# Optimization experiments

Hardware: AMD Instinct MI355X
Metric: run time of the kernel (lower is better)

The kernel has to match this reference:

```python
import jax, jax.numpy as jnp
import numpy as np

B, S, D = 2, 1024, 4096
HQ, HKV, HD = 32, 8, 128
GROUPS = HQ // HKV          # 4
SCALE = HD ** -0.5


def _rope_tables(key):
    # standard RoPE cos/sin tables, non-interleaved (half-split) layout
    inv_freq = 1.0 / (10000.0 ** (jnp.arange(0, HD, 2, dtype=jnp.float32) / HD))  # [HD/2]
    pos = jnp.arange(S, dtype=jnp.float32)                                        # [S]
    freqs = pos[:, None] * inv_freq[None, :]                                      # [S, HD/2]
    emb = jnp.concatenate([freqs, freqs], axis=-1)                                # [S, HD]
    cos = jnp.broadcast_to(jnp.cos(emb)[None], (B, S, HD))
    sin = jnp.broadcast_to(jnp.sin(emb)[None], (B, S, HD))
    return cos, sin


def setup_inputs() -> dict:
    key = jax.random.key(0)
    ks = jax.random.split(key, 6)
    hidden_states = jax.random.normal(ks[0], (B, S, D), dtype=jnp.float32)
    cos_table, sin_table = _rope_tables(ks[1])
    Wq = jax.random.normal(ks[2], (D, HQ * HD), dtype=jnp.float32) * (D ** -0.5)
    Wk = jax.random.normal(ks[3], (D, HKV * HD), dtype=jnp.float32) * (D ** -0.5)
    Wv = jax.random.normal(ks[4], (D, HKV * HD), dtype=jnp.float32) * (D ** -0.5)
    Wo = jax.random.normal(ks[5], (HQ * HD, D), dtype=jnp.float32) * ((HQ * HD) ** -0.5)
    return {"hidden_states": hidden_states, "cos_table": cos_table,
            "sin_table": sin_table, "Wq": Wq, "Wk": Wk, "Wv": Wv, "Wo": Wo}


def _rotate_half(x):
    x1, x2 = jnp.split(x, 2, axis=-1)
    return jnp.concatenate([-x2, x1], axis=-1)


def _apply_rope(x, cos, sin):
    # x: [B, S, H, HD]; cos/sin: [B, S, HD] broadcast across heads
    c = cos[:, :, None, :]
    s = sin[:, :, None, :]
    return x * c + _rotate_half(x) * s


def reference(hidden_states, cos_table, sin_table, Wq, Wk, Wv, Wo):
    b, s, _ = hidden_states.shape
    # QKV projections (no bias, Llama-style)
    q = (hidden_states @ Wq).reshape(b, s, HQ, HD)
    k = (hidden_states @ Wk).reshape(b, s, HKV, HD)
    v = (hidden_states @ Wv).reshape(b, s, HKV, HD)
    # fused RoPE on q and k (in [B, S, H, HD] layout, as in source)
    q = _apply_rope(q, cos_table, sin_table)
    k = _apply_rope(k, cos_table, sin_table)
    # -> [B, H, S, HD]
    q = q.transpose(0, 2, 1, 3)
    k = k.transpose(0, 2, 1, 3)
    v = v.transpose(0, 2, 1, 3)
    # GQA repeat_kv: [B, HKV, S, HD] -> [B, HQ, S, HD]
    k = jnp.repeat(k, GROUPS, axis=1)
    v = jnp.repeat(v, GROUPS, axis=1)
    # SDPA, no mask (source calls sdpa without a mask)
    scores = jnp.einsum('bhqd,bhkd->bhqk', q, k) * SCALE
    attn = jax.nn.softmax(scores, axis=-1)
    out = jnp.einsum('bhqk,bhkd->bhqd', attn, v)
    out = out.transpose(0, 2, 1, 3).reshape(b, s, HQ * HD)
    return out @ Wo
```

## Files before the change

### kernel.cpp

```cpp
#include <hip/hip_runtime.h>

#define B_   2
#define S_   1024
#define D_   4096
#define HQ_  32
#define HKV_ 8
#define HD_  128
#define SCALE_ 0.08838834764831845f

typedef unsigned short u16;
typedef __attribute__((ext_vector_type(8))) short s16x8;
typedef __attribute__((ext_vector_type(4))) short s16x4;
typedef __attribute__((ext_vector_type(4))) float f32x4;

#define MFMA(a,b,c) __builtin_amdgcn_mfma_f32_16x16x32_bf16((a),(b),(c),0,0,0)

__device__ __forceinline__ u16 bf16_rne(float x) {
  unsigned u = __float_as_uint(x);
  u += 0x7fffu + ((u >> 16) & 1u);
  return (u16)(u >> 16);
}
__device__ __forceinline__ float bf16_up(u16 h) {
  return __uint_as_float(((unsigned)h) << 16);
}
__device__ __forceinline__ void split2(float x, u16& h, u16& l) {
  h = bf16_rne(x);
  l = bf16_rne(x - bf16_up(h));
}

__device__ __forceinline__ void cvt_hi_lo(float a, float b, unsigned& hi, unsigned& lo) {
  unsigned h, l;
  asm("v_cvt_pk_bf16_f32 %0, %1, %2" : "=v"(h) : "v"(a), "v"(b));
  float ra = __uint_as_float(h << 16);
  float rb = __uint_as_float(h & 0xffff0000u);
  float la = a - ra, lb = b - rb;
  asm("v_cvt_pk_bf16_f32 %0, %1, %2" : "=v"(l) : "v"(la), "v"(lb));
  hi = h; lo = l;
}
__device__ __forceinline__ void pack8(float4 x, float4 y, uint4& h, uint4& l) {
  unsigned h0,h1,h2,h3,l0,l1,l2,l3;
  cvt_hi_lo(x.x, x.y, h0, l0);
  cvt_hi_lo(x.z, x.w, h1, l1);
  cvt_hi_lo(y.x, y.y, h2, l2);
  cvt_hi_lo(y.z, y.w, h3, l3);
  h = make_uint4(h0,h1,h2,h3); l = make_uint4(l0,l1,l2,l3);
}

typedef const __attribute__((address_space(1))) void* gas_ptr;
typedef __attribute__((address_space(3))) void* las_ptr;
__device__ __forceinline__ void gload_lds16(const void* g, void* l) {
  __builtin_amdgcn_global_load_lds((gas_ptr)g, (las_ptr)l, 16, 0, 0);
}

__global__ __launch_bounds__(256) void frag_b(
    const float* __restrict__ W, u16* __restrict__ dh, u16* __restrict__ dl,
    int N, int n0, int Nc16)
{
  __shared__ float T[32][68];
  const int kt = blockIdx.x, nbk = blockIdx.y;
  const int tid = threadIdx.x;
#pragma unroll
  for (int rep = 0; rep < 2; ++rep) {
    int idx = tid + rep * 256;
    int row = idx >> 4, c4 = (idx & 15) * 4;
    float4 v = *reinterpret_cast<const float4*>(&W[(size_t)(kt*32 + row) * N + n0 + nbk*64 + c4]);
    *reinterpret_cast<float4*>(&T[row][c4]) = v;
  }
  __syncthreads();
  const size_t base = ((size_t)kt * Nc16 + nbk * 4) * 512;
  int c = tid;
  int nt = c >> 6, l = c & 63, kc = l >> 4, r = l & 15;
  u16 hh[8], ll[8];
#pragma unroll
  for (int j = 0; j < 8; ++j) split2(T[kc*8 + j][nt*16 + r], hh[j], ll[j]);
  *reinterpret_cast<s16x8*>(&dh[base + (size_t)c * 8]) =
    (s16x8){(short)hh[0],(short)hh[1],(short)hh[2],(short)hh[3],
            (short)hh[4],(short)hh[5],(short)hh[6],(short)hh[7]};
  *reinterpret_cast<s16x8*>(&dl[base + (size_t)c * 8]) =
    (s16x8){(short)ll[0],(short)ll[1],(short)ll[2],(short)ll[3],
            (short)ll[4],(short)ll[5],(short)ll[6],(short)ll[7]};
}

__global__ __launch_bounds__(256) void frag_kv(
    const float* __restrict__ kb, const float* __restrict__ vb,
    u16* __restrict__ KFh, u16* __restrict__ KFl,
    u16* __restrict__ VFh, u16* __restrict__ VFl)
{
  __shared__ float T[32][132];
  const int bid  = blockIdx.x;
  const int isV  = bid >> 9;
  const int bkvh = (bid >> 5) & 15;
  const int chnk = bid & 31;
  const int tid  = threadIdx.x;
  const int b    = bkvh >> 3, kvh = bkvh & 7;

  const float* src = isV ? vb : kb;
  {
    int r0 = tid >> 5, c4 = (tid & 31) * 4;
#pragma unroll
    for (int it = 0; it < 4; ++it) {
      int row = r0 + it * 8;
      float4 v = *reinterpret_cast<const float4*>(
        &src[(((size_t)(b * S_ + chnk*32 + row)) * HKV_ + kvh) * HD_ + c4]);
      *reinterpret_cast<float4*>(&T[row][c4]) = v;
    }
  }
  __syncthreads();
#pragma unroll
  for (int rep = 0; rep < 2; ++rep) {
    int c2 = tid + rep * 256;
    int l = c2 & 63;
    u16 hh[8], ll[8];
    if (!isV) {
      int f = c2 >> 6, st_loc = f >> 2, dt = f & 3;
#pragma unroll
      for (int j = 0; j < 8; ++j)
        split2(T[st_loc*16 + (l & 15)][dt*32 + (l >> 4)*8 + j], hh[j], ll[j]);
      size_t off = ((size_t)bkvh*64 + chnk*2) * 2048 + (size_t)c2 * 8;
      *reinterpret_cast<s16x8*>(&KFh[off]) =
        (s16x8){(short)hh[0],(short)hh[1],(short)hh[2],(short)hh[3],
                (short)hh[4],(short)hh[5],(short)hh[6],(short)hh[7]};
      *reinterpret_cast<s16x8*>(&KFl[off]) =
        (s16x8){(short)ll[0],(short)ll[1],(short)ll[2],(short)ll[3],
                (short)ll[4],(short)ll[5],(short)ll[6],(short)ll[7]};
    } else {
      int dt16 = c2 >> 6;
#pragma unroll
      for (int j = 0; j < 8; ++j)
        split2(T[(l >> 4)*8 + j][dt16*16 + (l & 15)], hh[j], ll[j]);
      size_t off = ((size_t)bkvh*32 + chnk) * 4096 + (size_t)c2 * 8;
      *reinterpret_cast<s16x8*>(&VFh[off]) =
        (s16x8){(short)hh[0],(short)hh[1],(short)hh[2],(short)hh[3],
                (short)hh[4],(short)hh[5],(short)hh[6],(short)hh[7]};
      *reinterpret_cast<s16x8*>(&VFl[off]) =
        (s16x8){(short)ll[0],(short)ll[1],(short)ll[2],(short)ll[3],
                (short)ll[4],(short)ll[5],(short)ll[6],(short)ll[7]};
    }
  }
}

__global__ __launch_bounds__(512) void attn3(
    const float* __restrict__ qb,
    const u16* __restrict__ KFh, const u16* __restrict__ KFl,
    const u16* __restrict__ VFh, const u16* __restrict__ VFl,
    float* __restrict__ ob)
{
  __shared__ __attribute__((aligned(16))) u16 Klds[16384];
  __shared__ __attribute__((aligned(16))) u16 Vlds[16384];
  __shared__ u16 Ph[8][16][68], Pl[8][16][68];

  const int tid  = threadIdx.x;
  const int lane = tid & 63;
  const int wid  = tid >> 6;
  const int lr   = lane & 15;
  const int lg   = lane >> 4;
  const int loff = lane * 8;
  const int qt   = blockIdx.x;
  const int bh   = blockIdx.y;
  const int b    = bh >> 5, h = bh & 31;
  const int bkvh = b * 8 + (h >> 2);

  s16x8 qh[4], ql[4];
  {
    const int qrow = qt * 128 + wid * 16 + lr;
    const float* qp = qb + ((size_t)((b * S_ + qrow) * HQ_ + h)) * HD_;
#pragma unroll
    for (int kc = 0; kc < 4; ++kc) {
      const float* qp2 = qp + kc * 32 + lg * 8;
      float4 v0 = *reinterpret_cast<const float4*>(qp2);
      float4 v1 = *reinterpret_cast<const float4*>(qp2 + 4);
      uint4 h4, l4; pack8(v0, v1, h4, l4);
      qh[kc] = *reinterpret_cast<s16x8*>(&h4);
      ql[kc] = *reinterpret_cast<s16x8*>(&l4);
    }
  }

  f32x4 acc_o[8];
#pragma unroll
  for (int df = 0; df < 8; ++df) acc_o[df] = (f32x4){0.f, 0.f, 0.f, 0.f};
  float m_run[4] = {-1e30f, -1e30f, -1e30f, -1e30f};
  float l_run[4] = {0.f, 0.f, 0.f, 0.f};

  const u16* gKh = KFh + (size_t)bkvh * 131072;
  const u16* gKl = KFl + (size_t)bkvh * 131072;
  const u16* gVh = VFh + (size_t)bkvh * 131072;
  const u16* gVl = VFl + (size_t)bkvh * 131072;

#pragma unroll
  for (int i = 0; i < 4; ++i) {
    int idx = wid * 4 + i;
    const u16* src = (idx < 16) ? (gKh + idx*512) : (gKl + (idx-16)*512);
    u16* dst = Klds + ((idx < 16) ? idx*512 : 8192 + (idx-16)*512);
    gload_lds16(src + loff, dst);
  }
  __syncthreads();

  for (int t = 0; t < 16; ++t) {
#pragma unroll
    for (int i = 0; i < 4; ++i) {
      int idx = wid * 4 + i;
      const u16* src = (idx < 16) ? (gVh + t*8192 + idx*512)
                                  : (gVl + t*8192 + (idx-16)*512);
      u16* dst = Vlds + ((idx < 16) ? idx*512 : 8192 + (idx-16)*512);
      gload_lds16(src + loff, dst);
    }

    f32x4 accs[4];
#pragma unroll
    for (int nf = 0; nf < 4; ++nf) {
      accs[nf] = (f32x4){0.f, 0.f, 0.f, 0.f};
      s16x8 kh8[4], kl8[4];
#pragma unroll
      for (int kc = 0; kc < 4; ++kc) {
        kh8[kc] = *reinterpret_cast<const s16x8*>(&Klds[nf*2048 + kc*512 + loff]);
        kl8[kc] = *reinterpret_cast<const s16x8*>(&Klds[8192 + nf*2048 + kc*512 + loff]);
      }
#pragma unroll
      for (int kc = 0; kc < 4; ++kc) {
        accs[nf] = MFMA(qh[kc], kh8[kc], accs[nf]);
        accs[nf] = MFMA(ql[kc], kh8[kc], accs[nf]);
        accs[nf] = MFMA(qh[kc], kl8[kc], accs[nf]);
      }
    }
#pragma unroll
    for (int nf = 0; nf < 4; ++nf) accs[nf] *= SCALE_;

    float corr[4], rsum[4];
#pragma unroll
    for (int r = 0; r < 4; ++r) {
      float t0 = fmaxf(fmaxf(accs[0][r], accs[1][r]), fmaxf(accs[2][r], accs[3][r]));
      t0 = fmaxf(t0, __shfl_xor(t0, 1));
      t0 = fmaxf(t0, __shfl_xor(t0, 2));
      t0 = fmaxf(t0, __shfl_xor(t0, 4));
      t0 = fmaxf(t0, __shfl_xor(t0, 8));
      float mnew = fmaxf(m_run[r], t0);
      corr[r] = __expf(m_run[r] - mnew);
      m_run[r] = mnew;
      rsum[r] = 0.f;
    }
#pragma unroll
    for (int nf = 0; nf < 4; ++nf)
#pragma unroll
      for (int r = 0; r < 4; ++r) {
        float p = __expf(accs[nf][r] - m_run[r]);
        rsum[r] += p;
        u16 ph, pl;
        split2(p, ph, pl);
        Ph[wid][lg*4 + r][nf*16 + lr] = ph;
        Pl[wid][lg*4 + r][nf*16 + lr] = pl;
      }
#pragma unroll
    for (int r = 0; r < 4; ++r) {
      float s = rsum[r];
      s += __shfl_xor(s, 1); s += __shfl_xor(s, 2);
      s += __shfl_xor(s, 4); s += __shfl_xor(s, 8);
      l_run[r] = l_run[r] * corr[r] + s;
    }
#pragma unroll
    for (int df = 0; df < 8; ++df)
#pragma unroll
      for (int r = 0; r < 4; ++r) acc_o[df][r] *= corr[r];

    __syncthreads();

    if (t < 15) {
#pragma unroll
      for (int i = 0; i < 4; ++i) {
        int idx = wid * 4 + i;
        const u16* src = (idx < 16) ? (gKh + (t+1)*8192 + idx*512)
                                    : (gKl + (t+1)*8192 + (idx-16)*512);
        u16* dst = Klds + ((idx < 16) ? idx*512 : 8192 + (idx-16)*512);
        gload_lds16(src + loff, dst);
      }
    }

    s16x8 pa_h[2], pa_l[2];
#pragma unroll
    for (int kc = 0; kc < 2; ++kc) {
      pa_h[kc] = *reinterpret_cast<const s16x8*>(&Ph[wid][lr][kc*32 + lg*8]);
      pa_l[kc] = *reinterpret_cast<const s16x8*>(&Pl[wid][lr][kc*32 + lg*8]);
    }
#pragma unroll
    for (int df = 0; df < 8; ++df) {
      s16x8 vh8[2], vl8[2];
#pragma unroll
      for (int kc = 0; kc < 2; ++kc) {
        vh8[kc] = *reinterpret_cast<const s16x8*>(&Vlds[kc*4096 + df*512 + loff]);
        vl8[kc] = *reinterpret_cast<const s16x8*>(&Vlds[8192 + kc*4096 + df*512 + loff]);
      }
#pragma unroll
      for (int kc = 0; kc < 2; ++kc) {
        acc_o[df] = MFMA(pa_h[kc], vh8[kc], acc_o[df]);
        acc_o[df] = MFMA(pa_l[kc], vh8[kc], acc_o[df]);
        acc_o[df] = MFMA(pa_h[kc], vl8[kc], acc_o[df]);
      }
    }
    __syncthreads();
  }

  float inv_l[4];
#pragma unroll
  for (int r = 0; r < 4; ++r) inv_l[r] = 1.f / l_run[r];
#pragma unroll
  for (int df = 0; df < 8; ++df)
#pragma unroll
    for (int r = 0; r < 4; ++r) {
      int row = qt * 128 + wid * 16 + lg * 4 + r;
      ob[((size_t)((b * S_ + row) * HQ_ + h)) * HD_ + df*16 + lr] = acc_o[df][r] * inv_l[r];
    }
}

__global__ __launch_bounds__(512) void gemm_p1(
    const float* __restrict__ X, const float* __restrict__ abp,
    const u16* __restrict__ WF,
    float* __restrict__ qb, float* __restrict__ kb, float* __restrict__ vb,
    float* __restrict__ outp, int mode, int col0)
{
  __shared__ __attribute__((aligned(16))) u16 lds[40960];
  u16* ah0 = lds;
  u16* al0 = lds + 4096;
  u16* ah1 = lds + 8192;
  u16* al1 = lds + 12288;
  u16* bh0 = lds + 16384;
  u16* bh1 = lds + 24576;
  u16* blb = lds + 32768;

  const int id   = blockIdx.x;
  const int cpx  = gridDim.x >> 3;
  const int swz  = (id & 7) * cpx + (id >> 3);

  const float* A; const u16* Bh; const u16* Bl; float* C;
  int ldc, Nc16, mb, nb;
  if (mode == 0) {
    if (swz < 128)      { A=X; Bh=WF;          Bl=WF+8388608;  C=qb; ldc=4096; Nc16=128; mb=swz>>3; nb=swz&7; }
    else if (swz < 192) { int u=swz-128; A=X; Bh=WF+16777216; Bl=WF+20971520; C=kb; ldc=1024; Nc16=64; mb=u>>2; nb=u&3; }
    else                { int u=swz-192; A=X; Bh=WF+25165824; Bl=WF+29360128; C=vb; ldc=1024; Nc16=64; mb=u>>2; nb=u&3; }
  } else if (mode == 1) {
    A=X; Bh=WF; Bl=WF+8388608; C=qb+col0; ldc=4096; Nc16=128; mb=swz>>3; nb=swz&7;
  } else if (mode == 2) {
    if (swz < 64) { A=X; Bh=WF;          Bl=WF+4194304;  C=kb; ldc=1024; Nc16=64; mb=swz>>2; nb=swz&3; }
    else          { int u=swz-64; A=X; Bh=WF+8388608; Bl=WF+12582912; C=vb; ldc=1024; Nc16=64; mb=u>>2; nb=u&3; }
  } else if (mode == 3) {
    A=abp; Bh=WF; Bl=WF+16777216; C=outp; ldc=4096; Nc16=256; mb=swz>>4; nb=swz&15;
  } else {
    A=abp; Bh=WF; Bl=WF+8388608; C=outp+col0; ldc=4096; Nc16=128; mb=swz>>3; nb=swz&7;
  }

  const int tid  = threadIdx.x;
  const int lane = tid & 63;
  const int wid  = tid >> 6;
  const int mtb  = (wid >> 2) * 4;
  const int ntb  = (wid & 3) * 4;
  const int loff = lane * 8;

  const int arow = tid >> 2;
  const int akc  = tid & 3;
  const float* aptr = A + (size_t)(mb*128 + arow) * 4096 + akc*8;
  const int awr = (arow >> 4)*512 + (akc*16 + (arow & 15))*8;

  const size_t bStep = (size_t)Nc16 * 512;
  const u16* pBh = Bh + (size_t)nb*16*512 + loff;
  const u16* pBl = Bl + (size_t)nb*16*512 + loff;

  f32x4 acc[4][4];
#pragma unroll
  for (int i = 0; i < 4; ++i)
#pragma unroll
    for (int j = 0; j < 4; ++j) acc[i][j] = (f32x4){0.f, 0.f, 0.f, 0.f};

  float4 ra0 = *reinterpret_cast<const float4*>(aptr);
  float4 ra1 = *reinterpret_cast<const float4*>(aptr + 4);
  {
    uint4 h4, l4; pack8(ra0, ra1, h4, l4);
    *reinterpret_cast<uint4*>(&ah0[awr]) = h4;
    *reinterpret_cast<uint4*>(&al0[awr]) = l4;
  }
  gload_lds16(pBh + (size_t)wid*512,     bh0 + wid*512);
  gload_lds16(pBh + (size_t)(wid+8)*512, bh0 + (wid+8)*512);
  ra0 = *reinterpret_cast<const float4*>(aptr + 32);
  ra1 = *reinterpret_cast<const float4*>(aptr + 36);
  __syncthreads();

  for (int kt = 0; kt < 128; ++kt) {
    u16* cAh = (kt & 1) ? ah1 : ah0;
    u16* cAl = (kt & 1) ? al1 : al0;
    u16* nAh = (kt & 1) ? ah0 : ah1;
    u16* nAl = (kt & 1) ? al0 : al1;
    u16* cBh = (kt & 1) ? bh1 : bh0;
    u16* nBh = (kt & 1) ? bh0 : bh1;

    gload_lds16(pBl + (size_t)kt*bStep + (size_t)wid*512,     blb + wid*512);
    gload_lds16(pBl + (size_t)kt*bStep + (size_t)(wid+8)*512, blb + (wid+8)*512);
    if (kt < 127) {
      gload_lds16(pBh + (size_t)(kt+1)*bStep + (size_t)wid*512,     nBh + wid*512);
      gload_lds16(pBh + (size_t)(kt+1)*bStep + (size_t)(wid+8)*512, nBh + (wid+8)*512);
    }
    s16x8 a_h[4], a_l[4], b_h[4];
#pragma unroll
    for (int mf = 0; mf < 4; ++mf) {
      a_h[mf] = *reinterpret_cast<const s16x8*>(&cAh[(mtb+mf)*512 + loff]);
      a_l[mf] = *reinterpret_cast<const s16x8*>(&cAl[(mtb+mf)*512 + loff]);
    }
#pragma unroll
    for (int nf = 0; nf < 4; ++nf)
      b_h[nf] = *reinterpret_cast<const s16x8*>(&cBh[(ntb+nf)*512 + loff]);
#pragma unroll
    for (int mf = 0; mf < 4; ++mf)
#pragma unroll
      for (int nf = 0; nf < 4; ++nf) {
        acc[mf][nf] = MFMA(a_h[mf], b_h[nf], acc[mf][nf]);
        acc[mf][nf] = MFMA(a_l[mf], b_h[nf], acc[mf][nf]);
      }
    __syncthreads();

    s16x8 b_l[4];
#pragma unroll
    for (int nf = 0; nf < 4; ++nf)
      b_l[nf] = *reinterpret_cast<const s16x8*>(&blb[(ntb+nf)*512 + loff]);
#pragma unroll
    for (int mf = 0; mf < 4; ++mf)
#pragma unroll
      for (int nf = 0; nf < 4; ++nf)
        acc[mf][nf] = MFMA(a_h[mf], b_l[nf], acc[mf][nf]);
    if (kt < 127) {
      uint4 h4, l4; pack8(ra0, ra1, h4, l4);
      *reinterpret_cast<uint4*>(&nAh[awr]) = h4;
      *reinterpret_cast<uint4*>(&nAl[awr]) = l4;
      if (kt < 126) {
        ra0 = *reinterpret_cast<const float4*>(aptr + (kt+2)*32);
        ra1 = *reinterpret_cast<const float4*>(aptr + (kt+2)*32 + 4);
      }
    }
    __syncthreads();
  }

  const int lr = lane & 15, lg = lane >> 4;
  const int row0 = mb*128 + (wid >> 2) * 64;
  const int nloc = nb*256 + (wid & 3) * 64;
#pragma unroll
  for (int mf = 0; mf < 4; ++mf)
#pragma unroll
    for (int nf = 0; nf < 4; ++nf)
#pragma unroll
      for (int r = 0; r < 4; ++r)
        C[(size_t)(row0 + mf*16 + lg*4 + r) * ldc + nloc + nf*16 + lr] = acc[mf][nf][r];
}

__device__ __forceinline__ void gemm_core_128x256(
    const float* __restrict__ A, const float* __restrict__ W,
    float* __restrict__ C, int ldw, int m0, int n0)
{
  __shared__ u16 Ah[128][40];
  __shared__ u16 Al[128][40];
  __shared__ u16 Bh[256][40];
  __shared__ u16 Bl[256][40];

  const int tid  = threadIdx.x;
  const int lane = tid & 63;
  const int wid  = tid >> 6;
  const int wm   = (wid >> 2) * 64;
  const int wn   = (wid & 3) * 64;
  const int lr   = lane & 15;
  const int lg   = lane >> 4;

  f32x4 acc[4][4];
#pragma unroll
  for (int i = 0; i < 4; ++i)
#pragma unroll
    for (int j = 0; j < 4; ++j) acc[i][j] = (f32x4){0.f, 0.f, 0.f, 0.f};

  const int ar  = tid >> 3;
  const int ak  = (tid & 7) * 4;
  const int bn  = tid & 255;
  const int bk0 = (tid >> 8) * 16;

  for (int kt = 0; kt < D_ / 32; ++kt) {
    const int k0 = kt * 32;
    __syncthreads();
#pragma unroll
    for (int j = 0; j < 2; ++j) {
      int r = ar + 64 * j;
      float4 v = *reinterpret_cast<const float4*>(&A[(size_t)(m0 + r) * D_ + k0 + ak]);
      u16 h0,h1,h2,h3,l0,l1,l2,l3;
      split2(v.x,h0,l0); split2(v.y,h1,l1); split2(v.z,h2,l2); split2(v.w,h3,l3);
      *reinterpret_cast<s16x4*>(&Ah[r][ak]) = (s16x4){(short)h0,(short)h1,(short)h2,(short)h3};
      *reinterpret_cast<s16x4*>(&Al[r][ak]) = (s16x4){(short)l0,(short)l1,(short)l2,(short)l3};
    }
    {
      const float* wp = W + (size_t)(k0 + bk0) * ldw + (n0 + bn);
#pragma unroll
      for (int q = 0; q < 4; ++q) {
        float v0 = wp[(q*4 + 0) * (size_t)ldw];
        float v1 = wp[(q*4 + 1) * (size_t)ldw];
        float v2 = wp[(q*4 + 2) * (size_t)ldw];
        float v3 = wp[(q*4 + 3) * (size_t)ldw];
        u16 h0,h1,h2,h3,l0,l1,l2,l3;
        split2(v0,h0,l0); split2(v1,h1,l1); split2(v2,h2,l2); split2(v3,h3,l3);
        *reinterpret_cast<s16x4*>(&Bh[bn][bk0 + q*4]) = (s16x4){(short)h0,(short)h1,(short)h2,(short)h3};
        *reinterpret_cast<s16x4*>(&Bl[bn][bk0 + q*4]) = (s16x4){(short)l0,(short)l1,(short)l2,(short)l3};
      }
    }
    __syncthreads();
    s16x8 a_h[4], a_l[4], b_h[4], b_l[4];
#pragma unroll
    for (int mf = 0; mf < 4; ++mf) {
      a_h[mf] = *reinterpret_cast<const s16x8*>(&Ah[wm + mf*16 + lr][lg*8]);
      a_l[mf] = *reinterpret_cast<const s16x8*>(&Al[wm + mf*16 + lr][lg*8]);
    }
#pragma unroll
    for (int nf = 0; nf < 4; ++nf) {
      b_h[nf] = *reinterpret_cast<const s16x8*>(&Bh[wn + nf*16 + lr][lg*8]);
      b_l[nf] = *reinterpret_cast<const s16x8*>(&Bl[wn + nf*16 + lr][lg*8]);
    }
#pragma unroll
    for (int mf = 0; mf < 4; ++mf)
#pragma unroll
      for (int nf = 0; nf < 4; ++nf) {
        acc[mf][nf] = MFMA(a_h[mf], b_h[nf], acc[mf][nf]);
        acc[mf][nf] = MFMA(a_l[mf], b_h[nf], acc[mf][nf]);
        acc[mf][nf] = MFMA(a_h[mf], b_l[nf], acc[mf][nf]);
      }
  }
#pragma unroll
  for (int mf = 0; mf < 4; ++mf)
#pragma unroll
    for (int nf = 0; nf < 4; ++nf)
#pragma unroll
      for (int r = 0; r < 4; ++r) {
        int row = m0 + wm + mf*16 + lg*4 + r;
        int col = n0 + wn + nf*16 + lr;
        C[(size_t)row * ldw + col] = acc[mf][nf][r];
      }
}

__global__ __launch_bounds__(512) void gemm_qkv_kernel(
    const float* __restrict__ X,
    const float* __restrict__ Wq, const float* __restrict__ Wk,
    const float* __restrict__ Wv,
    float* __restrict__ qb, float* __restrict__ kb, float* __restrict__ vb)
{
  int nbv = blockIdx.x;
  int m0 = blockIdx.y * 128;
  const float* W; float* C; int ldw, n0;
  if (nbv < 16)      { W = Wq; C = qb; ldw = HQ_*HD_;  n0 = nbv * 256; }
  else if (nbv < 20) { W = Wk; C = kb; ldw = HKV_*HD_; n0 = (nbv-16) * 256; }
  else               { W = Wv; C = vb; ldw = HKV_*HD_; n0 = (nbv-20) * 256; }
  gemm_core_128x256(X, W, C, ldw, m0, n0);
}

__global__ __launch_bounds__(512) void gemm_out_kernel(
    const float* __restrict__ A, const float* __restrict__ Wo, float* __restrict__ out)
{
  gemm_core_128x256(A, Wo, out, D_, blockIdx.y * 128, blockIdx.x * 256);
}

__global__ __launch_bounds__(256) void rope_kernel(
    float* __restrict__ qb, float* __restrict__ kb,
    const float* __restrict__ cosT, const float* __restrict__ sinT)
{
  int idx = blockIdx.x * 256 + threadIdx.x;
  const int nq = B_ * S_ * HQ_ * (HD_/2);
  const int nk = B_ * S_ * HKV_ * (HD_/2);
  if (idx < nq) {
    int j = idx & 63;
    int h = (idx >> 6) & (HQ_ - 1);
    int bs = idx >> 11;
    float* p = qb + ((size_t)bs * HQ_ + h) * HD_;
    const float* cp = cosT + (size_t)bs * HD_;
    const float* sp = sinT + (size_t)bs * HD_;
    float x1 = p[j], x2 = p[j + 64];
    p[j]      = x1 * cp[j]      - x2 * sp[j];
    p[j + 64] = x2 * cp[j + 64] + x1 * sp[j + 64];
  } else if (idx < nq + nk) {
    int t2 = idx - nq;
    int j = t2 & 63;
    int h = (t2 >> 6) & (HKV_ - 1);
    int bs = t2 >> 9;
    float* p = kb + ((size_t)bs * HKV_ + h) * HD_;
    const float* cp = cosT + (size_t)bs * HD_;
    const float* sp = sinT + (size_t)bs * HD_;
    float x1 = p[j], x2 = p[j + 64];
    p[j]      = x1 * cp[j]      - x2 * sp[j];
    p[j + 64] = x2 * cp[j + 64] + x1 * sp[j + 64];
  }
}

__global__ __launch_bounds__(512) void attn_kernel(
    const float* __restrict__ qb, const float* __restrict__ kb,
    const float* __restrict__ vb, float* __restrict__ ob)
{
  __shared__ u16 Kh[64][136], Kl[64][136];
  __shared__ u16 Vh[128][72], Vl[128][72];
  __shared__ u16 Ph[8][16][72], Pl[8][16][72];

  const int tid  = threadIdx.x;
  const int lane = tid & 63;
  const int wid  = tid >> 6;
  const int lr   = lane & 15;
  const int lg   = lane >> 4;
  const int qt   = blockIdx.x;
  const int bh   = blockIdx.y;
  const int b    = bh >> 5, h = bh & 31, kvh = h >> 2;

  s16x8 qh[4], ql[4];
  {
    const int qrow = qt * 128 + wid * 16 + lr;
    const float* qp = qb + ((size_t)((b * S_ + qrow) * HQ_ + h)) * HD_;
#pragma unroll
    for (int kc = 0; kc < 4; ++kc) {
      const float* qp2 = qp + kc * 32 + lg * 8;
      float4 v0 = *reinterpret_cast<const float4*>(qp2);
      float4 v1 = *reinterpret_cast<const float4*>(qp2 + 4);
      u16 hh[8], ll[8];
      split2(v0.x,hh[0],ll[0]); split2(v0.y,hh[1],ll[1]);
      split2(v0.z,hh[2],ll[2]); split2(v0.w,hh[3],ll[3]);
      split2(v1.x,hh[4],ll[4]); split2(v1.y,hh[5],ll[5]);
      split2(v1.z,hh[6],ll[6]); split2(v1.w,hh[7],ll[7]);
      qh[kc] = (s16x8){(short)hh[0],(short)hh[1],(short)hh[2],(short)hh[3],
                       (short)hh[4],(short)hh[5],(short)hh[6],(short)hh[7]};
      ql[kc] = (s16x8){(short)ll[0],(short)ll[1],(short)ll[2],(short)ll[3],
                       (short)ll[4],(short)ll[5],(short)ll[6],(short)ll[7]};
    }
  }

  f32x4 acc_o[8];
#pragma unroll
  for (int df = 0; df < 8; ++df) acc_o[df] = (f32x4){0.f, 0.f, 0.f, 0.f};
  float m_run[4] = {-1e30f, -1e30f, -1e30f, -1e30f};
  float l_run[4] = {0.f, 0.f, 0.f, 0.f};

  const float* kbase = kb + ((size_t)(b * S_) * HKV_ + kvh) * HD_;
  const float* vbase = vb + ((size_t)(b * S_) * HKV_ + kvh) * HD_;

  for (int t = 0; t < S_ / 64; ++t) {
    const int kk0 = t * 64;
    __syncthreads();
#pragma unroll
    for (int j = 0; j < 4; ++j) {
      int idx = tid + 512 * j;
      int kk = idx >> 5, dq = (idx & 31) * 4;
      float4 v = *reinterpret_cast<const float4*>(kbase + (size_t)(kk0 + kk) * (HKV_*HD_) + dq);
      u16 h0,h1,h2,h3,l0,l1,l2,l3;
      split2(v.x,h0,l0); split2(v.y,h1,l1); split2(v.z,h2,l2); split2(v.w,h3,l3);
      *reinterpret_cast<s16x4*>(&Kh[kk][dq]) = (s16x4){(short)h0,(short)h1,(short)h2,(short)h3};
      *reinterpret_cast<s16x4*>(&Kl[kk][dq]) = (s16x4){(short)l0,(short)l1,(short)l2,(short)l3};
    }
    {
      int d = tid & 127;
      int kkb = (tid >> 7) * 16;
      const float* vcol = vbase + d;
#pragma unroll
      for (int jq = 0; jq < 4; ++jq) {
        u16 h4[4], l4[4];
#pragma unroll
        for (int e = 0; e < 4; ++e) {
          float val = vcol[(size_t)(kk0 + kkb + jq*4 + e) * (HKV_*HD_)];
          split2(val, h4[e], l4[e]);
        }
        *reinterpret_cast<s16x4*>(&Vh[d][kkb + jq*4]) = (s16x4){(short)h4[0],(short)h4[1],(short)h4[2],(short)h4[3]};
        *reinterpret_cast<s16x4*>(&Vl[d][kkb + jq*4]) = (s16x4){(short)l4[0],(short)l4[1],(short)l4[2],(short)l4[3]};
      }
    }
    __syncthreads();
    f32x4 accs[4];
#pragma unroll
    for (int nf = 0; nf < 4; ++nf) accs[nf] = (f32x4){0.f, 0.f, 0.f, 0.f};
#pragma unroll
    for (int nf = 0; nf < 4; ++nf) {
      int krow = nf * 16 + lr;
#pragma unroll
      for (int kc = 0; kc < 4; ++kc) {
        s16x8 kh8 = *reinterpret_cast<const s16x8*>(&Kh[krow][kc*32 + lg*8]);
        s16x8 kl8 = *reinterpret_cast<const s16x8*>(&Kl[krow][kc*32 + lg*8]);
        accs[nf] = MFMA(qh[kc], kh8, accs[nf]);
        accs[nf] = MFMA(ql[kc], kh8, accs[nf]);
        accs[nf] = MFMA(qh[kc], kl8, accs[nf]);
      }
    }
#pragma unroll
    for (int nf = 0; nf < 4; ++nf) accs[nf] *= SCALE_;
    float corr[4], rsum[4];
#pragma unroll
    for (int r = 0; r < 4; ++r) {
      float t0 = fmaxf(fmaxf(accs[0][r], accs[1][r]), fmaxf(accs[2][r], accs[3][r]));
      t0 = fmaxf(t0, __shfl_xor(t0, 1));
      t0 = fmaxf(t0, __shfl_xor(t0, 2));
      t0 = fmaxf(t0, __shfl_xor(t0, 4));
      t0 = fmaxf(t0, __shfl_xor(t0, 8));
      float mnew = fmaxf(m_run[r], t0);
      corr[r] = __expf(m_run[r] - mnew);
      m_run[r] = mnew;
      rsum[r] = 0.f;
    }
#pragma unroll
    for (int nf = 0; nf < 4; ++nf)
#pragma unroll
      for (int r = 0; r < 4; ++r) {
        float p = __expf(accs[nf][r] - m_run[r]);
        rsum[r] += p;
        u16 ph, pl;
        split2(p, ph, pl);
        Ph[wid][lg*4 + r][nf*16 + lr] = ph;
        Pl[wid][lg*4 + r][nf*16 + lr] = pl;
      }
#pragma unroll
    for (int r = 0; r < 4; ++r) {
      float s = rsum[r];
      s += __shfl_xor(s, 1); s += __shfl_xor(s, 2);
      s += __shfl_xor(s, 4); s += __shfl_xor(s, 8);
      l_run[r] = l_run[r] * corr[r] + s;
    }
#pragma unroll
    for (int df = 0; df < 8; ++df)
#pragma unroll
      for (int r = 0; r < 4; ++r) acc_o[df][r] *= corr[r];
    s16x8 pa_h[2], pa_l[2];
#pragma unroll
    for (int kc = 0; kc < 2; ++kc) {
      pa_h[kc] = *reinterpret_cast<const s16x8*>(&Ph[wid][lr][kc*32 + lg*8]);
      pa_l[kc] = *reinterpret_cast<const s16x8*>(&Pl[wid][lr][kc*32 + lg*8]);
    }
#pragma unroll
    for (int df = 0; df < 8; ++df) {
      int dcol = df * 16 + lr;
#pragma unroll
      for (int kc = 0; kc < 2; ++kc) {
        s16x8 vh8 = *reinterpret_cast<const s16x8*>(&Vh[dcol][kc*32 + lg*8]);
        s16x8 vl8 = *reinterpret_cast<const s16x8*>(&Vl[dcol][kc*32 + lg*8]);
        acc_o[df] = MFMA(pa_h[kc], vh8, acc_o[df]);
        acc_o[df] = MFMA(pa_l[kc], vh8, acc_o[df]);
        acc_o[df] = MFMA(pa_h[kc], vl8, acc_o[df]);
      }
    }
  }
  float inv_l[4];
#pragma unroll
  for (int r = 0; r < 4; ++r) inv_l[r] = 1.f / l_run[r];
#pragma unroll
  for (int df = 0; df < 8; ++df)
#pragma unroll
    for (int r = 0; r < 4; ++r) {
      int row = qt * 128 + wid * 16 + lg * 4 + r;
      ob[((size_t)((b * S_ + row) * HQ_ + h)) * HD_ + df*16 + lr] = acc_o[df][r] * inv_l[r];
    }
}

extern "C" void kernel_launch(void* const* d_in, const int* in_sizes, int n_in,
                              void* d_out, int out_size, void* d_ws, size_t ws_size,
                              hipStream_t stream)
{
  const float* hs   = (const float*)d_in[0];
  const float* cosT = (const float*)d_in[1];
  const float* sinT = (const float*)d_in[2];
  const float* Wq   = (const float*)d_in[3];
  const float* Wk   = (const float*)d_in[4];
  const float* Wv   = (const float*)d_in[5];
  const float* Wo   = (const float*)d_in[6];
  float* out = (float*)d_out;

  float* qb = (float*)d_ws;
  float* kb = qb + 8388608;
  float* vb = kb + 2097152;
  float* ab = vb + 2097152;
  u16*   WF = (u16*)(ab + 8388608);

  const size_t WS144 = 83886080ULL + 67108864ULL;
  const size_t WS112 = 83886080ULL + 33554432ULL;
  int total = B_*S_*HQ_*(HD_/2) + B_*S_*HKV_*(HD_/2);

  u16* KFh = WF;
  u16* KFl = WF + 2097152;
  u16* VFh = WF + 4194304;
  u16* VFl = WF + 6291456;

  if (ws_size >= WS144) {
    frag_b<<<dim3(128,32), 256, 0, stream>>>(Wq, WF,          WF+8388608,  4096, 0,    128);
    frag_b<<<dim3(128,16), 256, 0, stream>>>(Wk, WF+16777216, WF+20971520, 1024, 0,    64);
    frag_b<<<dim3(128,16), 256, 0, stream>>>(Wv, WF+25165824, WF+29360128, 1024, 0,    64);
    gemm_p1<<<256, 512, 0, stream>>>(hs, ab, WF, qb, kb, vb, out, 0, 0);
    frag_b<<<dim3(128,32), 256, 0, stream>>>(Wq, WF,          WF+8388608,  4096, 2048, 128);
    gemm_p1<<<128, 512, 0, stream>>>(hs, ab, WF, qb, kb, vb, out, 1, 2048);
    rope_kernel<<<dim3((total + 255)/256), 256, 0, stream>>>(qb, kb, cosT, sinT);
    frag_kv<<<1024, 256, 0, stream>>>(kb, vb, KFh, KFl, VFh, VFl);
    attn3<<<dim3(8, 64), 512, 0, stream>>>(qb, KFh, KFl, VFh, VFl, ab);
    frag_b<<<dim3(128,64), 256, 0, stream>>>(Wo, WF,          WF+16777216, 4096, 0,    256);
    gemm_p1<<<256, 512, 0, stream>>>(hs, ab, WF, qb, kb, vb, out, 3, 0);
  } else if (ws_size >= WS112) {
    frag_b<<<dim3(128,32), 256, 0, stream>>>(Wq, WF, WF+8388608, 4096, 0, 128);
    gemm_p1<<<128, 512, 0, stream>>>(hs, ab, WF, qb, kb, vb, out, 1, 0);
    frag_b<<<dim3(128,32), 256, 0, stream>>>(Wq, WF, WF+8388608, 4096, 2048, 128);
    gemm_p1<<<128, 512, 0, stream>>>(hs, ab, WF, qb, kb, vb, out, 1, 2048);
    frag_b<<<dim3(128,16), 256, 0, stream>>>(Wk, WF,           WF+4194304,  1024, 0, 64);
    frag_b<<<dim3(128,16), 256, 0, stream>>>(Wv, WF+8388608,   WF+12582912, 1024, 0, 64);
    gemm_p1<<<128, 512, 0, stream>>>(hs, ab, WF, qb, kb, vb, out, 2, 0);
    rope_kernel<<<dim3((total + 255)/256), 256, 0, stream>>>(qb, kb, cosT, sinT);
    frag_kv<<<1024, 256, 0, stream>>>(kb, vb, KFh, KFl, VFh, VFl);
    attn3<<<dim3(8, 64), 512, 0, stream>>>(qb, KFh, KFl, VFh, VFl, ab);
    frag_b<<<dim3(128,32), 256, 0, stream>>>(Wo, WF, WF+8388608, 4096, 0, 128);
    gemm_p1<<<128, 512, 0, stream>>>(hs, ab, WF, qb, kb, vb, out, 4, 0);
    frag_b<<<dim3(128,32), 256, 0, stream>>>(Wo, WF, WF+8388608, 4096, 2048, 128);
    gemm_p1<<<128, 512, 0, stream>>>(hs, ab, WF, qb, kb, vb, out, 4, 2048);
  } else {
    gemm_qkv_kernel<<<dim3(24, 16), 512, 0, stream>>>(hs, Wq, Wk, Wv, qb, kb, vb);
    rope_kernel<<<dim3((total + 255)/256), 256, 0, stream>>>(qb, kb, cosT, sinT);
    attn_kernel<<<dim3(8, 64), 512, 0, stream>>>(qb, kb, vb, ab);
    gemm_out_kernel<<<dim3(16, 16), 512, 0, stream>>>(ab, Wo, out);
  }
}
```

Baseline: 734.3 us.

## Fuse RoPE into KV fragmenting and attention Q load, merge QKV GEMM launches

Removes the standalone RoPE kernel by applying the rotation when K is loaded into frag_kv and when Q is loaded in attn3, reading cos/sin tables directly. Adds a larger-workspace path that pre-fragments all of Wq, Wk and Wv up front and runs a single 384-block QKV GEMM (new mode 5) instead of two GEMM launches. Also swizzles the A-tile LDS layout in gemm_p1 to reduce bank conflicts. The cost is extra global loads of cos/sin and of the partner half inside attention and frag_kv, plus a larger workspace requirement for the new path.

```diff
diff --git a/kernel.cpp b/kernel.cpp
--- a/kernel.cpp
+++ b/kernel.cpp
@@ -83,6 +83,7 @@
 
 __global__ __launch_bounds__(256) void frag_kv(
     const float* __restrict__ kb, const float* __restrict__ vb,
+    const float* __restrict__ cosT, const float* __restrict__ sinT,
     u16* __restrict__ KFh, u16* __restrict__ KFl,
     u16* __restrict__ VFh, u16* __restrict__ VFl)
 {
@@ -97,11 +98,22 @@
   const float* src = isV ? vb : kb;
   {
     int r0 = tid >> 5, c4 = (tid & 31) * 4;
+    float sgn = (c4 < 64) ? -1.f : 1.f;
 #pragma unroll
     for (int it = 0; it < 4; ++it) {
       int row = r0 + it * 8;
-      float4 v = *reinterpret_cast<const float4*>(
-        &src[(((size_t)(b * S_ + chnk*32 + row)) * HKV_ + kvh) * HD_ + c4]);
+      int srow = chnk*32 + row;
+      const float* rp = &src[(((size_t)(b * S_ + srow)) * HKV_ + kvh) * HD_];
+      float4 v = *reinterpret_cast<const float4*>(rp + c4);
+      if (!isV) {
+        float4 p  = *reinterpret_cast<const float4*>(rp + (c4 ^ 64));
+        float4 cc = *reinterpret_cast<const float4*>(&cosT[((size_t)(b*S_ + srow))*HD_ + c4]);
+        float4 ss = *reinterpret_cast<const float4*>(&sinT[((size_t)(b*S_ + srow))*HD_ + c4]);
+        v.x = v.x*cc.x + sgn*p.x*ss.x;
+        v.y = v.y*cc.y + sgn*p.y*ss.y;
+        v.z = v.z*cc.z + sgn*p.z*ss.z;
+        v.w = v.w*cc.w + sgn*p.w*ss.w;
+      }
       *reinterpret_cast<float4*>(&T[row][c4]) = v;
     }
   }
@@ -141,6 +153,7 @@
 
 __global__ __launch_bounds__(512) void attn3(
     const float* __restrict__ qb,
+    const float* __restrict__ cosT, const float* __restrict__ sinT,
     const u16* __restrict__ KFh, const u16* __restrict__ KFl,
     const u16* __restrict__ VFh, const u16* __restrict__ VFl,
     float* __restrict__ ob)
@@ -164,12 +177,26 @@
   {
     const int qrow = qt * 128 + wid * 16 + lr;
     const float* qp = qb + ((size_t)((b * S_ + qrow) * HQ_ + h)) * HD_;
+    const float* cp = cosT + ((size_t)(b * S_ + qrow)) * HD_;
+    const float* sp = sinT + ((size_t)(b * S_ + qrow)) * HD_;
 #pragma unroll
     for (int kc = 0; kc < 4; ++kc) {
-      const float* qp2 = qp + kc * 32 + lg * 8;
-      float4 v0 = *reinterpret_cast<const float4*>(qp2);
-      float4 v1 = *reinterpret_cast<const float4*>(qp2 + 4);
-      uint4 h4, l4; pack8(v0, v1, h4, l4);
+      const int d0 = kc * 32 + lg * 8;
+      const float sgn = (d0 < 64) ? -1.f : 1.f;
+      float4 v0 = *reinterpret_cast<const float4*>(qp + d0);
+      float4 v1 = *reinterpret_cast<const float4*>(qp + d0 + 4);
+      float4 p0 = *reinterpret_cast<const float4*>(qp + (d0 ^ 64));
+      float4 p1 = *reinterpret_cast<const float4*>(qp + (d0 ^ 64) + 4);
+      float4 c0 = *reinterpret_cast<const float4*>(cp + d0);
+      float4 c1 = *reinterpret_cast<const float4*>(cp + d0 + 4);
+      float4 s0 = *reinterpret_cast<const float4*>(sp + d0);
+      float4 s1 = *reinterpret_cast<const float4*>(sp + d0 + 4);
+      float4 r0, r1;
+      r0.x = v0.x*c0.x + sgn*p0.x*s0.x;  r0.y = v0.y*c0.y + sgn*p0.y*s0.y;
+      r0.z = v0.z*c0.z + sgn*p0.z*s0.z;  r0.w = v0.w*c0.w + sgn*p0.w*s0.w;
+      r1.x = v1.x*c1.x + sgn*p1.x*s1.x;  r1.y = v1.y*c1.y + sgn*p1.y*s1.y;
+      r1.z = v1.z*c1.z + sgn*p1.z*s1.z;  r1.w = v1.w*c1.w + sgn*p1.w*s1.w;
+      uint4 h4, l4; pack8(r0, r1, h4, l4);
       qh[kc] = *reinterpret_cast<s16x8*>(&h4);
       ql[kc] = *reinterpret_cast<s16x8*>(&l4);
     }
@@ -342,8 +369,13 @@
     else          { int u=swz-64; A=X; Bh=WF+8388608; Bl=WF+12582912; C=vb; ldc=1024; Nc16=64; mb=u>>2; nb=u&3; }
   } else if (mode == 3) {
     A=abp; Bh=WF; Bl=WF+16777216; C=outp; ldc=4096; Nc16=256; mb=swz>>4; nb=swz&15;
+  } else if (mode == 4) {
+    A=abp; Bh=WF; Bl=WF+8388608; C=outp+col0; ldc=4096; Nc16=128; mb=swz>>3; nb=swz&7;
   } else {
-    A=abp; Bh=WF; Bl=WF+8388608; C=outp+col0; ldc=4096; Nc16=128; mb=swz>>3; nb=swz&7;
+    if (swz < 128)      { A=X; Bh=WF;          Bl=WF+8388608;  C=qb;      ldc=4096; Nc16=128; mb=swz>>3; nb=swz&7; }
+    else if (swz < 256) { int u=swz-128; A=X; Bh=WF+16777216; Bl=WF+25165824; C=qb+2048; ldc=4096; Nc16=128; mb=u>>3; nb=u&7; }
+    else if (swz < 320) { int u=swz-256; A=X; Bh=WF+33554432; Bl=WF+37748736; C=kb; ldc=1024; Nc16=64; mb=u>>2; nb=u&3; }
+    else                { int u=swz-320; A=X; Bh=WF+41943040; Bl=WF+46137344; C=vb; ldc=1024; Nc16=64; mb=u>>2; nb=u&3; }
   }
 
   const int tid  = threadIdx.x;
@@ -352,11 +384,14 @@
   const int mtb  = (wid >> 2) * 4;
   const int ntb  = (wid & 3) * 4;
   const int loff = lane * 8;
+  const int lg   = lane >> 4;
+  const int lr_  = lane & 15;
+  const int aoff = (lg*16 + ((lr_ + 4*lg) & 15)) * 8;
 
   const int arow = tid >> 2;
   const int akc  = tid & 3;
   const float* aptr = A + (size_t)(mb*128 + arow) * 4096 + akc*8;
-  const int awr = (arow >> 4)*512 + (akc*16 + (arow & 15))*8;
+  const int awr = (arow >> 4)*512 + (akc*16 + (((arow & 15) + 4*akc) & 15))*8;
 
   const size_t bStep = (size_t)Nc16 * 512;
   const u16* pBh = Bh + (size_t)nb*16*512 + loff;
@@ -398,8 +433,8 @@
     s16x8 a_h[4], a_l[4], b_h[4];
 #pragma unroll
     for (int mf = 0; mf < 4; ++mf) {
-      a_h[mf] = *reinterpret_cast<const s16x8*>(&cAh[(mtb+mf)*512 + loff]);
-      a_l[mf] = *reinterpret_cast<const s16x8*>(&cAl[(mtb+mf)*512 + loff]);
+      a_h[mf] = *reinterpret_cast<const s16x8*>(&cAh[(mtb+mf)*512 + aoff]);
+      a_l[mf] = *reinterpret_cast<const s16x8*>(&cAl[(mtb+mf)*512 + aoff]);
     }
 #pragma unroll
     for (int nf = 0; nf < 4; ++nf)
@@ -434,7 +469,6 @@
     __syncthreads();
   }
 
-  const int lr = lane & 15, lg = lane >> 4;
   const int row0 = mb*128 + (wid >> 2) * 64;
   const int nloc = nb*256 + (wid & 3) * 64;
 #pragma unroll
@@ -443,7 +477,7 @@
     for (int nf = 0; nf < 4; ++nf)
 #pragma unroll
       for (int r = 0; r < 4; ++r)
-        C[(size_t)(row0 + mf*16 + lg*4 + r) * ldc + nloc + nf*16 + lr] = acc[mf][nf][r];
+        C[(size_t)(row0 + mf*16 + lg*4 + r) * ldc + nloc + nf*16 + lr_] = acc[mf][nf][r];
 }
 
 __device__ __forceinline__ void gemm_core_128x256(
@@ -764,8 +798,9 @@
   float* ab = vb + 2097152;
   u16*   WF = (u16*)(ab + 8388608);
 
-  const size_t WS144 = 83886080ULL + 67108864ULL;
-  const size_t WS112 = 83886080ULL + 33554432ULL;
+  const size_t WS185 = 184549376ULL;
+  const size_t WS144 = 150994944ULL;
+  const size_t WS112 = 117440512ULL;
   int total = B_*S_*HQ_*(HD_/2) + B_*S_*HKV_*(HD_/2);
 
   u16* KFh = WF;
@@ -773,16 +808,25 @@
   u16* VFh = WF + 4194304;
   u16* VFl = WF + 6291456;
 
-  if (ws_size >= WS144) {
+  if (ws_size >= WS185) {
+    frag_b<<<dim3(128,32), 256, 0, stream>>>(Wq, WF,          WF+8388608,  4096, 0,    128);
+    frag_b<<<dim3(128,32), 256, 0, stream>>>(Wq, WF+16777216, WF+25165824, 4096, 2048, 128);
+    frag_b<<<dim3(128,16), 256, 0, stream>>>(Wk, WF+33554432, WF+37748736, 1024, 0,    64);
+    frag_b<<<dim3(128,16), 256, 0, stream>>>(Wv, WF+41943040, WF+46137344, 1024, 0,    64);
+    gemm_p1<<<384, 512, 0, stream>>>(hs, ab, WF, qb, kb, vb, out, 5, 0);
+    frag_kv<<<1024, 256, 0, stream>>>(kb, vb, cosT, sinT, KFh, KFl, VFh, VFl);
+    attn3<<<dim3(8, 64), 512, 0, stream>>>(qb, cosT, sinT, KFh, KFl, VFh, VFl, ab);
+    frag_b<<<dim3(128,64), 256, 0, stream>>>(Wo, WF, WF+16777216, 4096, 0, 256);
+    gemm_p1<<<256, 512, 0, stream>>>(hs, ab, WF, qb, kb, vb, out, 3, 0);
+  } else if (ws_size >= WS144) {
     frag_b<<<dim3(128,32), 256, 0, stream>>>(Wq, WF,          WF+8388608,  4096, 0,    128);
     frag_b<<<dim3(128,16), 256, 0, stream>>>(Wk, WF+16777216, WF+20971520, 1024, 0,    64);
     frag_b<<<dim3(128,16), 256, 0, stream>>>(Wv, WF+25165824, WF+29360128, 1024, 0,    64);
     gemm_p1<<<256, 512, 0, stream>>>(hs, ab, WF, qb, kb, vb, out, 0, 0);
     frag_b<<<dim3(128,32), 256, 0, stream>>>(Wq, WF,          WF+8388608,  4096, 2048, 128);
     gemm_p1<<<128, 512, 0, stream>>>(hs, ab, WF, qb, kb, vb, out, 1, 2048);
-    rope_kernel<<<dim3((total + 255)/256), 256, 0, stream>>>(qb, kb, cosT, sinT);
-    frag_kv<<<1024, 256, 0, stream>>>(kb, vb, KFh, KFl, VFh, VFl);
-    attn3<<<dim3(8, 64), 512, 0, stream>>>(qb, KFh, KFl, VFh, VFl, ab);
+    frag_kv<<<1024, 256, 0, stream>>>(kb, vb, cosT, sinT, KFh, KFl, VFh, VFl);
+    attn3<<<dim3(8, 64), 512, 0, stream>>>(qb, cosT, sinT, KFh, KFl, VFh, VFl, ab);
     frag_b<<<dim3(128,64), 256, 0, stream>>>(Wo, WF,          WF+16777216, 4096, 0,    256);
     gemm_p1<<<256, 512, 0, stream>>>(hs, ab, WF, qb, kb, vb, out, 3, 0);
   } else if (ws_size >= WS112) {
@@ -793,9 +837,8 @@
     frag_b<<<dim3(128,16), 256, 0, stream>>>(Wk, WF,           WF+4194304,  1024, 0, 64);
     frag_b<<<dim3(128,16), 256, 0, stream>>>(Wv, WF+8388608,   WF+12582912, 1024, 0, 64);
     gemm_p1<<<128, 512, 0, stream>>>(hs, ab, WF, qb, kb, vb, out, 2, 0);
-    rope_kernel<<<dim3((total + 255)/256), 256, 0, stream>>>(qb, kb, cosT, sinT);
-    frag_kv<<<1024, 256, 0, stream>>>(kb, vb, KFh, KFl, VFh, VFl);
-    attn3<<<dim3(8, 64), 512, 0, stream>>>(qb, KFh, KFl, VFh, VFl, ab);
+    frag_kv<<<1024, 256, 0, stream>>>(kb, vb, cosT, sinT, KFh, KFl, VFh, VFl);
+    attn3<<<dim3(8, 64), 512, 0, stream>>>(qb, cosT, sinT, KFh, KFl, VFh, VFl, ab);
     frag_b<<<dim3(128,32), 256, 0, stream>>>(Wo, WF, WF+8388608, 4096, 0, 128);
     gemm_p1<<<128, 512, 0, stream>>>(hs, ab, WF, qb, kb, vb, out, 4, 0);
     frag_b<<<dim3(128,32), 256, 0, stream>>>(Wo, WF, WF+8388608, 4096, 2048, 128);
```

Result: faster. 712.6 us (-3.0%).
